# Optimization experiments

Measured on AMD Instinct MI355X. Metric: run time of the kernel, lower is better.

## Reference

```python
import jax, jax.numpy as jnp
import numpy as np

N_NODES = 50000
N_EDGES = 640000
D = 128      # in_feats
OUT = 128    # out_feats


def setup_inputs() -> dict:
    key = jax.random.key(0)
    ks = jax.random.split(key, 8)
    feat = jax.random.normal(ks[0], (N_NODES, D), dtype=jnp.float32)
    weight = jax.random.uniform(ks[1], (N_EDGES,), dtype=jnp.float32)
    src = jax.random.randint(ks[2], (N_EDGES,), 0, N_NODES, dtype=jnp.int64)
    dst = jax.random.randint(ks[3], (N_EDGES,), 0, N_NODES, dtype=jnp.int64)
    # xavier_uniform with relu gain ~ sqrt(2)*sqrt(6/(fan_in+fan_out))
    g = np.sqrt(2.0)
    lim_pool = g * np.sqrt(6.0 / (D + D))
    lim_neigh = g * np.sqrt(6.0 / (2 * D + OUT))
    W_pool = jax.random.uniform(ks[4], (D, D), dtype=jnp.float32, minval=-lim_pool, maxval=lim_pool)
    b_pool = jnp.zeros((D,), dtype=jnp.float32)
    W_neigh = jax.random.uniform(ks[5], (OUT, 2 * D), dtype=jnp.float32, minval=-lim_neigh, maxval=lim_neigh)
    b_neigh = jnp.zeros((OUT,), dtype=jnp.float32)
    return {"feat": feat, "weight": weight, "src": src, "dst": dst,
            "W_pool": W_pool, "b_pool": b_pool, "W_neigh": W_neigh, "b_neigh": b_neigh}


def reference(feat, weight, src, dst, W_pool, b_pool, W_neigh, b_neigh):
    n = feat.shape[0]
    # fc_pool: h = feat @ W_pool.T + b_pool  -> [N, D]
    h = feat @ W_pool.T + b_pool
    # u_mul_e: per-edge message m_e = h[src_e] * w_e  -> [E, D]
    m = h[src] * weight[:, None]
    # max reduce over incoming edges (scatter-max by dst)
    neigh = jax.ops.segment_max(m, dst, num_segments=n)
    # zero-degree nodes get 0 (segment_max fills empties with -inf)
    deg = jax.ops.segment_sum(jnp.ones_like(weight), dst, num_segments=n)
    neigh = jnp.where(deg[:, None] > 0, neigh, jnp.zeros((), dtype=feat.dtype))
    # fc_neigh on concat(feat, neigh)
    rst = jnp.concatenate([feat, neigh], axis=1) @ W_neigh.T + b_neigh
    return rst
```

## Files before the change

### kernel.cpp

```cpp
#include <hip/hip_runtime.h>
#include <cstdint>
#include <cstddef>

#define N_NODES 50000
#define N_EDGES 640000
#define DF 128

#define NBUCK 196
#define BCAP  6144
#define PA_BLOCKS 250

typedef __attribute__((ext_vector_type(8))) short bf16x8;
typedef __attribute__((ext_vector_type(4))) float f32x4;

__device__ inline unsigned short f2bf(float f) {
    unsigned int u = __float_as_uint(f);
    return (unsigned short)((u + 0x7fffu + ((u >> 16) & 1u)) >> 16);
}

#define NF4 (N_NODES * DF / 4)
#define NWG (3 * 2048)
__global__ __launch_bounds__(256) void k1_setup_bucket(
    const float* __restrict__ feat,
    const float* __restrict__ W_pool,
    const float* __restrict__ W_neigh,
    const int* __restrict__ src,
    const int* __restrict__ dst,
    const float* __restrict__ w,
    unsigned short* __restrict__ featb,
    unsigned short* __restrict__ Wp_f,
    unsigned short* __restrict__ Wn1_f,
    unsigned short* __restrict__ Wn2_f,
    int* __restrict__ bucketcnt,
    uint2* __restrict__ staging)
{
    int bid = blockIdx.x;
    int t = threadIdx.x;
    if (bid < PA_BLOCKS) {
        __shared__ int cnt[NBUCK];
        __shared__ int runbase[NBUCK];
        int base = bid * 2560;
        if (t < NBUCK) cnt[t] = 0;
        __syncthreads();
        uint2 rec[10];
        int bk[10];
        #pragma unroll
        for (int i = 0; i < 10; ++i) {
            int e = base + i * 256 + t;
            int s = src[e], d = dst[e];
            bk[i] = d >> 8;
            rec[i].x = (unsigned int)s | ((unsigned int)(d & 255) << 16);
            rec[i].y = __float_as_uint(w[e]);
            atomicAdd(&cnt[bk[i]], 1);
        }
        __syncthreads();
        if (t < NBUCK) {
            runbase[t] = atomicAdd(&bucketcnt[t], cnt[t]);
            cnt[t] = 0;
        }
        __syncthreads();
        #pragma unroll
        for (int i = 0; i < 10; ++i) {
            int r = atomicAdd(&cnt[bk[i]], 1);
            int pos = runbase[bk[i]] + r;
            if (pos < BCAP) staging[bk[i] * BCAP + pos] = rec[i];
        }
    } else if (bid < 250 + NF4 / 256) {
        int idx = (bid - PA_BLOCKS) * 256 + t;
        float4 v = ((const float4*)feat)[idx];
        ushort4 o;
        o.x = f2bf(v.x); o.y = f2bf(v.y); o.z = f2bf(v.z); o.w = f2bf(v.w);
        ((ushort4*)featb)[idx] = o;
    } else {
        int g = (bid - PA_BLOCKS - NF4 / 256) * 256 + t;
        int m = g >> 11;
        int r8 = g & 2047;
        int L = r8 & 63, tt = (r8 >> 6) & 3, c = r8 >> 8;
        int o = c * 16 + (L & 15);
        int kb = tt * 32 + (L >> 4) * 8;
        const float* srcp;
        unsigned short* dstp;
        if (m == 0)      { srcp = W_pool  + o * 128 + kb;       dstp = Wp_f;  }
        else if (m == 1) { srcp = W_neigh + o * 256 + kb;       dstp = Wn1_f; }
        else             { srcp = W_neigh + o * 256 + 128 + kb; dstp = Wn2_f; }
        ushort4 lo, hi;
        float4 a = ((const float4*)srcp)[0];
        float4 b = ((const float4*)srcp)[1];
        lo.x = f2bf(a.x); lo.y = f2bf(a.y); lo.z = f2bf(a.z); lo.w = f2bf(a.w);
        hi.x = f2bf(b.x); hi.y = f2bf(b.y); hi.z = f2bf(b.z); hi.w = f2bf(b.w);
        ((ushort4*)(dstp + r8 * 8))[0] = lo;
        ((ushort4*)(dstp + r8 * 8))[1] = hi;
    }
}

#define GEMMB 196
__global__ __launch_bounds__(1024) void k2_gemm_passb(
    const unsigned short* __restrict__ featb,
    const unsigned short* __restrict__ Wp_f,
    const float* __restrict__ b_pool,
    unsigned short* __restrict__ hb,
    const int* __restrict__ bucketcnt,
    const uint2* __restrict__ staging,
    int* __restrict__ offsets,
    uint2* __restrict__ edges)
{
    int t = threadIdx.x;
    if (blockIdx.x < GEMMB) {
        int wave = blockIdx.x * 16 + (t >> 6);
        int lane = t & 63;
        int m0 = wave * 16;
        if (m0 >= N_NODES) return;
        const int n = lane & 15, quad = lane >> 4;

        f32x4 acc[8];
        #pragma unroll
        for (int c = 0; c < 8; ++c) {
            float bv = b_pool[c * 16 + n];
            acc[c] = (f32x4){bv, bv, bv, bv};
        }
        const unsigned short* aptr = featb + (size_t)(m0 + n) * DF + quad * 8;
        #pragma unroll
        for (int tt = 0; tt < 4; ++tt) {
            bf16x8 af = *(const bf16x8*)(aptr + tt * 32);
            #pragma unroll
            for (int c = 0; c < 8; ++c) {
                bf16x8 bf = *(const bf16x8*)(Wp_f + (size_t)((c * 4 + tt) * 64 + lane) * 8);
                acc[c] = __builtin_amdgcn_mfma_f32_16x16x32_bf16(af, bf, acc[c], 0, 0, 0);
            }
        }
        #pragma unroll
        for (int c = 0; c < 8; ++c)
            #pragma unroll
            for (int r = 0; r < 4; ++r)
                hb[(size_t)(m0 + quad * 4 + r) * DF + c * 16 + n] = f2bf(acc[c][r]);
    } else {
        __shared__ int dcnt[256];
        __shared__ int sc[256];
        __shared__ int bc[256];
        int b = blockIdx.x - GEMMB;

        if (t < 256) { dcnt[t] = 0; bc[t] = (t < NBUCK) ? bucketcnt[t] : 0; sc[t] = (t < NBUCK) ? bc[t] : 0; }
        __syncthreads();
        #pragma unroll
        for (int off = 1; off < 256; off <<= 1) {
            int u = (t < 256 && t >= off) ? sc[t - off] : 0;
            __syncthreads();
            if (t < 256) sc[t] += u;
            __syncthreads();
        }
        int mybase = (b > 0) ? sc[b - 1] : 0;
        int cnt = bc[b];
        __syncthreads();

        uint2 rec[6];
        int nit = (cnt + 1023) >> 10;
        for (int i = 0; i < nit; ++i) {
            int idx = i * 1024 + t;
            if (idx < cnt) {
                rec[i] = staging[(size_t)b * BCAP + idx];
                atomicAdd(&dcnt[(rec[i].x >> 16) & 255], 1);
            }
        }
        __syncthreads();
        if (t < 256) sc[t] = dcnt[t];
        __syncthreads();
        #pragma unroll
        for (int off = 1; off < 256; off <<= 1) {
            int u = (t < 256 && t >= off) ? sc[t - off] : 0;
            __syncthreads();
            if (t < 256) sc[t] += u;
            __syncthreads();
        }
        if (t < 256) {
            int node = b * 256 + t;
            int excl = sc[t] - dcnt[t];
            if (node < N_NODES) offsets[node] = mybase + excl;
            dcnt[t] = mybase + excl;
        }
        if (b == NBUCK - 1 && t == 0) offsets[N_NODES] = mybase + cnt;
        __syncthreads();
        for (int i = 0; i < nit; ++i) {
            int idx = i * 1024 + t;
            if (idx < cnt) {
                int dl = (rec[i].x >> 16) & 255;
                int pos = atomicAdd(&dcnt[dl], 1);
                uint2 fin;
                fin.x = rec[i].x & 0xFFFFu;
                fin.y = rec[i].y;
                edges[pos] = fin;
            }
        }
    }
}

__global__ __launch_bounds__(256) void fused_max_out(
    const unsigned short* __restrict__ featb,
    const unsigned short* __restrict__ hb,
    const int* __restrict__ offsets,
    const uint2* __restrict__ edges,
    const unsigned short* __restrict__ Wn1_f,
    const unsigned short* __restrict__ Wn2_f,
    const float* __restrict__ bias,
    float* __restrict__ out)
{
    __shared__ __align__(16) unsigned short nsh[16 * DF];
    const int t = threadIdx.x;
    const int lane = t & 63;
    const int m0 = blockIdx.x * 16;
    const int half = lane >> 5;
    const int q = lane & 31;

    #pragma unroll 1
    for (int j = 0; j < 4; ++j) {
        const int row = ((t >> 6) << 2) + j;
        const int node = __builtin_amdgcn_readfirstlane(m0 + row);
        int beg = offsets[node], end = offsets[node + 1];
        float4 mx = make_float4(-3.4e38f, -3.4e38f, -3.4e38f, -3.4e38f);

        for (int e = beg; e < end; e += 8) {
            int i1 = min(e + 1, end - 1);
            int i2 = min(e + 2, end - 1);
            int i3 = min(e + 3, end - 1);
            int i4 = min(e + 4, end - 1);
            int i5 = min(e + 5, end - 1);
            int i6 = min(e + 6, end - 1);
            int i7 = min(e + 7, end - 1);
            uint2 e0 = edges[e],  e1 = edges[i1], e2 = edges[i2], e3 = edges[i3];
            uint2 e4 = edges[i4], e5 = edges[i5], e6 = edges[i6], e7 = edges[i7];
            uint2 mA = half ? e1 : e0;
            uint2 mB = half ? e3 : e2;
            uint2 mC = half ? e5 : e4;
            uint2 mD = half ? e7 : e6;
            float wA = __uint_as_float(mA.y);
            float wB = __uint_as_float(mB.y);
            float wC = __uint_as_float(mC.y);
            float wD = __uint_as_float(mD.y);
            uint2 pA = *(const uint2*)(hb + (size_t)mA.x * DF + q * 4);
            uint2 pB = *(const uint2*)(hb + (size_t)mB.x * DF + q * 4);
            uint2 pC = *(const uint2*)(hb + (size_t)mC.x * DF + q * 4);
            uint2 pD = *(const uint2*)(hb + (size_t)mD.x * DF + q * 4);
            mx.x = fmaxf(mx.x, __uint_as_float(pA.x << 16)          * wA);
            mx.y = fmaxf(mx.y, __uint_as_float(pA.x & 0xffff0000u)  * wA);
            mx.z = fmaxf(mx.z, __uint_as_float(pA.y << 16)          * wA);
            mx.w = fmaxf(mx.w, __uint_as_float(pA.y & 0xffff0000u)  * wA);
            mx.x = fmaxf(mx.x, __uint_as_float(pB.x << 16)          * wB);
            mx.y = fmaxf(mx.y, __uint_as_float(pB.x & 0xffff0000u)  * wB);
            mx.z = fmaxf(mx.z, __uint_as_float(pB.y << 16)          * wB);
            mx.w = fmaxf(mx.w, __uint_as_float(pB.y & 0xffff0000u)  * wB);
            mx.x = fmaxf(mx.x, __uint_as_float(pC.x << 16)          * wC);
            mx.y = fmaxf(mx.y, __uint_as_float(pC.x & 0xffff0000u)  * wC);
            mx.z = fmaxf(mx.z, __uint_as_float(pC.y << 16)          * wC);
            mx.w = fmaxf(mx.w, __uint_as_float(pC.y & 0xffff0000u)  * wC);
            mx.x = fmaxf(mx.x, __uint_as_float(pD.x << 16)          * wD);
            mx.y = fmaxf(mx.y, __uint_as_float(pD.x & 0xffff0000u)  * wD);
            mx.z = fmaxf(mx.z, __uint_as_float(pD.y << 16)          * wD);
            mx.w = fmaxf(mx.w, __uint_as_float(pD.y & 0xffff0000u)  * wD);
        }

        float4 o;
        o.x = fmaxf(mx.x, __shfl_xor(mx.x, 32));
        o.y = fmaxf(mx.y, __shfl_xor(mx.y, 32));
        o.z = fmaxf(mx.z, __shfl_xor(mx.z, 32));
        o.w = fmaxf(mx.w, __shfl_xor(mx.w, 32));
        if (beg == end) o = make_float4(0.f, 0.f, 0.f, 0.f);
        if (half == 0) {
            ushort4 ob;
            ob.x = f2bf(o.x); ob.y = f2bf(o.y); ob.z = f2bf(o.z); ob.w = f2bf(o.w);
            int boff = row * 256 + ((q * 8) ^ ((row & 7) << 4));
            *(ushort4*)((char*)nsh + boff) = ob;
        }
    }

    const int n = lane & 15, quad = lane >> 4;
    f32x4 acc[8];
    #pragma unroll
    for (int c = 0; c < 8; ++c) {
        float bv = bias[c * 16 + n];
        acc[c] = (f32x4){bv, bv, bv, bv};
    }

    const unsigned short* a0 = featb + (size_t)(m0 + n) * DF + quad * 8;
    #pragma unroll
    for (int tt = 0; tt < 4; ++tt) {
        bf16x8 af = *(const bf16x8*)(a0 + tt * 32);
        #pragma unroll
        for (int c = 0; c < 8; ++c) {
            bf16x8 bfv = *(const bf16x8*)(Wn1_f + (size_t)((c * 4 + tt) * 64 + lane) * 8);
            acc[c] = __builtin_amdgcn_mfma_f32_16x16x32_bf16(af, bfv, acc[c], 0, 0, 0);
        }
    }

    __syncthreads();

    #pragma unroll
    for (int tt = 0; tt < 4; ++tt) {
        int boff = (quad * 16 + tt * 64) ^ ((n & 7) << 4);
        bf16x8 af = *(const bf16x8*)((const char*)nsh + n * 256 + boff);
        #pragma unroll
        for (int c = 0; c < 8; ++c) {
            bf16x8 bfv = *(const bf16x8*)(Wn2_f + (size_t)((c * 4 + tt) * 64 + lane) * 8);
            acc[c] = __builtin_amdgcn_mfma_f32_16x16x32_bf16(af, bfv, acc[c], 0, 0, 0);
        }
    }

    #pragma unroll
    for (int c = 0; c < 8; ++c)
        #pragma unroll
        for (int r = 0; r < 4; ++r)
            out[(size_t)(m0 + quad * 4 + r) * DF + c * 16 + n] = acc[c][r];
}

extern "C" void kernel_launch(void* const* d_in, const int* in_sizes, int n_in,
                              void* d_out, int out_size, void* d_ws, size_t ws_size,
                              hipStream_t stream) {
    const float* feat    = (const float*)d_in[0];
    const float* weight  = (const float*)d_in[1];
    const int*   src     = (const int*)d_in[2];
    const int*   dst     = (const int*)d_in[3];
    const float* W_pool  = (const float*)d_in[4];
    const float* b_pool  = (const float*)d_in[5];
    const float* W_neigh = (const float*)d_in[6];
    const float* b_neigh = (const float*)d_in[7];
    float* out = (float*)d_out;

    char* ws = (char*)d_ws;
    unsigned short* featb  = (unsigned short*)(ws);
    unsigned short* hb     = (unsigned short*)(ws + 12800000);
    unsigned short* Wp_f   = (unsigned short*)(ws + 38400000);
    unsigned short* Wn1_f  = (unsigned short*)(ws + 38432768);
    unsigned short* Wn2_f  = (unsigned short*)(ws + 38465536);
    int*   offsets   = (int*)  (ws + 38498304);
    int*   bucketcnt = (int*)  (ws + 38698368);
    uint2* staging   = (uint2*)(ws + 38699392);
    uint2* edges     = (uint2*)(ws + 48333184);

    hipMemsetAsync(bucketcnt, 0, 1024, stream);

    const int K1_BLOCKS = PA_BLOCKS + NF4 / 256 + NWG / 256;
    k1_setup_bucket<<<K1_BLOCKS, 256, 0, stream>>>(
        feat, W_pool, W_neigh, src, dst, weight,
        featb, Wp_f, Wn1_f, Wn2_f, bucketcnt, staging);

    k2_gemm_passb<<<GEMMB + NBUCK, 1024, 0, stream>>>(
        featb, Wp_f, b_pool, hb, bucketcnt, staging, offsets, edges);

    fused_max_out<<<N_NODES / 16, 256, 0, stream>>>(
        featb, hb, offsets, edges, Wn1_f, Wn2_f, b_neigh, out);
}
```

Baseline: 193.5 us.

## Use one wave per node in fused max-aggregate kernel with 1024-thread blocks

The fused gather-max/output kernel now launches 1024-thread blocks so each of the 16 waves handles one destination node's max aggregation, where before each wave looped over four nodes. The output GEMM is split so that the first 8 waves each compute one 16-column tile of the output, while the other waves exit after the barrier. This exposes more memory-level parallelism in the irregular gather and shortens the serial per-wave loop. The cost is idle waves during the MFMA phase and larger blocks, which may limit occupancy and scheduling flexibility.

Result: faster. 163.4 us (-15.6%).

```diff
diff --git a/kernel.cpp b/kernel.cpp
--- a/kernel.cpp
+++ b/kernel.cpp
@@ -193,7 +193,7 @@
     }
 }
 
-__global__ __launch_bounds__(256) void fused_max_out(
+__global__ __launch_bounds__(1024) void fused_max_out(
     const unsigned short* __restrict__ featb,
     const unsigned short* __restrict__ hb,
     const int* __restrict__ offsets,
@@ -206,108 +206,98 @@
     __shared__ __align__(16) unsigned short nsh[16 * DF];
     const int t = threadIdx.x;
     const int lane = t & 63;
+    const int wid = t >> 6;
     const int m0 = blockIdx.x * 16;
     const int half = lane >> 5;
     const int q = lane & 31;
 
-    #pragma unroll 1
-    for (int j = 0; j < 4; ++j) {
-        const int row = ((t >> 6) << 2) + j;
-        const int node = __builtin_amdgcn_readfirstlane(m0 + row);
-        int beg = offsets[node], end = offsets[node + 1];
-        float4 mx = make_float4(-3.4e38f, -3.4e38f, -3.4e38f, -3.4e38f);
-
-        for (int e = beg; e < end; e += 8) {
-            int i1 = min(e + 1, end - 1);
-            int i2 = min(e + 2, end - 1);
-            int i3 = min(e + 3, end - 1);
-            int i4 = min(e + 4, end - 1);
-            int i5 = min(e + 5, end - 1);
-            int i6 = min(e + 6, end - 1);
-            int i7 = min(e + 7, end - 1);
-            uint2 e0 = edges[e],  e1 = edges[i1], e2 = edges[i2], e3 = edges[i3];
-            uint2 e4 = edges[i4], e5 = edges[i5], e6 = edges[i6], e7 = edges[i7];
-            uint2 mA = half ? e1 : e0;
-            uint2 mB = half ? e3 : e2;
-            uint2 mC = half ? e5 : e4;
-            uint2 mD = half ? e7 : e6;
-            float wA = __uint_as_float(mA.y);
-            float wB = __uint_as_float(mB.y);
-            float wC = __uint_as_float(mC.y);
-            float wD = __uint_as_float(mD.y);
-            uint2 pA = *(const uint2*)(hb + (size_t)mA.x * DF + q * 4);
-            uint2 pB = *(const uint2*)(hb + (size_t)mB.x * DF + q * 4);
-            uint2 pC = *(const uint2*)(hb + (size_t)mC.x * DF + q * 4);
-            uint2 pD = *(const uint2*)(hb + (size_t)mD.x * DF + q * 4);
-            mx.x = fmaxf(mx.x, __uint_as_float(pA.x << 16)          * wA);
-            mx.y = fmaxf(mx.y, __uint_as_float(pA.x & 0xffff0000u)  * wA);
-            mx.z = fmaxf(mx.z, __uint_as_float(pA.y << 16)          * wA);
-            mx.w = fmaxf(mx.w, __uint_as_float(pA.y & 0xffff0000u)  * wA);
-            mx.x = fmaxf(mx.x, __uint_as_float(pB.x << 16)          * wB);
-            mx.y = fmaxf(mx.y, __uint_as_float(pB.x & 0xffff0000u)  * wB);
-            mx.z = fmaxf(mx.z, __uint_as_float(pB.y << 16)          * wB);
-            mx.w = fmaxf(mx.w, __uint_as_float(pB.y & 0xffff0000u)  * wB);
-            mx.x = fmaxf(mx.x, __uint_as_float(pC.x << 16)          * wC);
-            mx.y = fmaxf(mx.y, __uint_as_float(pC.x & 0xffff0000u)  * wC);
-            mx.z = fmaxf(mx.z, __uint_as_float(pC.y << 16)          * wC);
-            mx.w = fmaxf(mx.w, __uint_as_float(pC.y & 0xffff0000u)  * wC);
-            mx.x = fmaxf(mx.x, __uint_as_float(pD.x << 16)          * wD);
-            mx.y = fmaxf(mx.y, __uint_as_float(pD.x & 0xffff0000u)  * wD);
-            mx.z = fmaxf(mx.z, __uint_as_float(pD.y << 16)          * wD);
-            mx.w = fmaxf(mx.w, __uint_as_float(pD.y & 0xffff0000u)  * wD);
-        }
-
-        float4 o;
-        o.x = fmaxf(mx.x, __shfl_xor(mx.x, 32));
-        o.y = fmaxf(mx.y, __shfl_xor(mx.y, 32));
-        o.z = fmaxf(mx.z, __shfl_xor(mx.z, 32));
-        o.w = fmaxf(mx.w, __shfl_xor(mx.w, 32));
-        if (beg == end) o = make_float4(0.f, 0.f, 0.f, 0.f);
-        if (half == 0) {
-            ushort4 ob;
-            ob.x = f2bf(o.x); ob.y = f2bf(o.y); ob.z = f2bf(o.z); ob.w = f2bf(o.w);
-            int boff = row * 256 + ((q * 8) ^ ((row & 7) << 4));
-            *(ushort4*)((char*)nsh + boff) = ob;
-        }
+    const int node = __builtin_amdgcn_readfirstlane(m0 + wid);
+    int beg = offsets[node], end = offsets[node + 1];
+    float4 mx = make_float4(-3.4e38f, -3.4e38f, -3.4e38f, -3.4e38f);
+
+    for (int e = beg; e < end; e += 8) {
+        int i1 = min(e + 1, end - 1);
+        int i2 = min(e + 2, end - 1);
+        int i3 = min(e + 3, end - 1);
+        int i4 = min(e + 4, end - 1);
+        int i5 = min(e + 5, end - 1);
+        int i6 = min(e + 6, end - 1);
+        int i7 = min(e + 7, end - 1);
+        uint2 e0 = edges[e],  e1 = edges[i1], e2 = edges[i2], e3 = edges[i3];
+        uint2 e4 = edges[i4], e5 = edges[i5], e6 = edges[i6], e7 = edges[i7];
+        uint2 mA = half ? e1 : e0;
+        uint2 mB = half ? e3 : e2;
+        uint2 mC = half ? e5 : e4;
+        uint2 mD = half ? e7 : e6;
+        float wA = __uint_as_float(mA.y);
+        float wB = __uint_as_float(mB.y);
+        float wC = __uint_as_float(mC.y);
+        float wD = __uint_as_float(mD.y);
+        uint2 pA = *(const uint2*)(hb + (size_t)mA.x * DF + q * 4);
+        uint2 pB = *(const uint2*)(hb + (size_t)mB.x * DF + q * 4);
+        uint2 pC = *(const uint2*)(hb + (size_t)mC.x * DF + q * 4);
+        uint2 pD = *(const uint2*)(hb + (size_t)mD.x * DF + q * 4);
+        mx.x = fmaxf(mx.x, __uint_as_float(pA.x << 16)          * wA);
+        mx.y = fmaxf(mx.y, __uint_as_float(pA.x & 0xffff0000u)  * wA);
+        mx.z = fmaxf(mx.z, __uint_as_float(pA.y << 16)          * wA);
+        mx.w = fmaxf(mx.w, __uint_as_float(pA.y & 0xffff0000u)  * wA);
+        mx.x = fmaxf(mx.x, __uint_as_float(pB.x << 16)          * wB);
+        mx.y = fmaxf(mx.y, __uint_as_float(pB.x & 0xffff0000u)  * wB);
+        mx.z = fmaxf(mx.z, __uint_as_float(pB.y << 16)          * wB);
+        mx.w = fmaxf(mx.w, __uint_as_float(pB.y & 0xffff0000u)  * wB);
+        mx.x = fmaxf(mx.x, __uint_as_float(pC.x << 16)          * wC);
+        mx.y = fmaxf(mx.y, __uint_as_float(pC.x & 0xffff0000u)  * wC);
+        mx.z = fmaxf(mx.z, __uint_as_float(pC.y << 16)          * wC);
+        mx.w = fmaxf(mx.w, __uint_as_float(pC.y & 0xffff0000u)  * wC);
+        mx.x = fmaxf(mx.x, __uint_as_float(pD.x << 16)          * wD);
+        mx.y = fmaxf(mx.y, __uint_as_float(pD.x & 0xffff0000u)  * wD);
+        mx.z = fmaxf(mx.z, __uint_as_float(pD.y << 16)          * wD);
+        mx.w = fmaxf(mx.w, __uint_as_float(pD.y & 0xffff0000u)  * wD);
+    }
+
+    float4 o;
+    o.x = fmaxf(mx.x, __shfl_xor(mx.x, 32));
+    o.y = fmaxf(mx.y, __shfl_xor(mx.y, 32));
+    o.z = fmaxf(mx.z, __shfl_xor(mx.z, 32));
+    o.w = fmaxf(mx.w, __shfl_xor(mx.w, 32));
+    if (beg == end) o = make_float4(0.f, 0.f, 0.f, 0.f);
+    if (half == 0) {
+        ushort4 ob;
+        ob.x = f2bf(o.x); ob.y = f2bf(o.y); ob.z = f2bf(o.z); ob.w = f2bf(o.w);
+        int boff = wid * 256 + ((q * 8) ^ ((wid & 7) << 4));
+        *(ushort4*)((char*)nsh + boff) = ob;
     }
 
     const int n = lane & 15, quad = lane >> 4;
-    f32x4 acc[8];
-    #pragma unroll
-    for (int c = 0; c < 8; ++c) {
+    f32x4 acc;
+    if (wid < 8) {
+        const int c = wid;
         float bv = bias[c * 16 + n];
-        acc[c] = (f32x4){bv, bv, bv, bv};
-    }
-
-    const unsigned short* a0 = featb + (size_t)(m0 + n) * DF + quad * 8;
-    #pragma unroll
-    for (int tt = 0; tt < 4; ++tt) {
-        bf16x8 af = *(const bf16x8*)(a0 + tt * 32);
-        #pragma unroll
-        for (int c = 0; c < 8; ++c) {
+        acc = (f32x4){bv, bv, bv, bv};
+        const unsigned short* a0 = featb + (size_t)(m0 + n) * DF + quad * 8;
+        #pragma unroll
+        for (int tt = 0; tt < 4; ++tt) {
+            bf16x8 af = *(const bf16x8*)(a0 + tt * 32);
             bf16x8 bfv = *(const bf16x8*)(Wn1_f + (size_t)((c * 4 + tt) * 64 + lane) * 8);
-            acc[c] = __builtin_amdgcn_mfma_f32_16x16x32_bf16(af, bfv, acc[c], 0, 0, 0);
+            acc = __builtin_amdgcn_mfma_f32_16x16x32_bf16(af, bfv, acc, 0, 0, 0);
         }
     }
 
     __syncthreads();
-
+    if (wid >= 8) return;
+
+    const int c = wid;
     #pragma unroll
     for (int tt = 0; tt < 4; ++tt) {
         int boff = (quad * 16 + tt * 64) ^ ((n & 7) << 4);
         bf16x8 af = *(const bf16x8*)((const char*)nsh + n * 256 + boff);
-        #pragma unroll
-        for (int c = 0; c < 8; ++c) {
-            bf16x8 bfv = *(const bf16x8*)(Wn2_f + (size_t)((c * 4 + tt) * 64 + lane) * 8);
-            acc[c] = __builtin_amdgcn_mfma_f32_16x16x32_bf16(af, bfv, acc[c], 0, 0, 0);
-        }
+        bf16x8 bfv = *(const bf16x8*)(Wn2_f + (size_t)((c * 4 + tt) * 64 + lane) * 8);
+        acc = __builtin_amdgcn_mfma_f32_16x16x32_bf16(af, bfv, acc, 0, 0, 0);
     }
 
     #pragma unroll
-    for (int c = 0; c < 8; ++c)
-        #pragma unroll
-        for (int r = 0; r < 4; ++r)
-            out[(size_t)(m0 + quad * 4 + r) * DF + c * 16 + n] = acc[c][r];
+    for (int r = 0; r < 4; ++r)
+        out[(size_t)(m0 + quad * 4 + r) * DF + c * 16 + n] = acc[r];
 }
 
 extern "C" void kernel_launch(void* const* d_in, const int* in_sizes, int n_in,
@@ -344,6 +334,6 @@
     k2_gemm_passb<<<GEMMB + NBUCK, 1024, 0, stream>>>(
         featb, Wp_f, b_pool, hb, bucketcnt, staging, offsets, edges);
 
-    fused_max_out<<<N_NODES / 16, 256, 0, stream>>>(
+    fused_max_out<<<N_NODES / 16, 1024, 0, stream>>>(
         featb, hb, offsets, edges, Wn1_f, Wn2_f, b_neigh, out);
 }
```

## Pad per-node edge lists to multiples of 8 and split max-aggregation from output GEMM

Applied to the files above, without the earlier changes.

Each node's edge list is padded to a multiple of 8 with dummy edges that point at a sentinel hb row holding a very negative value. This removes the per-iteration min() index clamping in the gather loop. Buckets get a fixed ECAP-sized edge region, so the cross-bucket prefix scan is no longer needed. The fused max+GEMM kernel is split into a one-wave-per-node max kernel that writes a bf16 neigh buffer, followed by a separate MFMA GEMM kernel. The split adds an extra launch plus a round trip of the neigh buffer through global memory, and padding adds gather traffic on the sentinel row.

Measured after the change: 162.3 us. 16.1% less time.

```diff
diff --git a/kernel.cpp b/kernel.cpp
--- a/kernel.cpp
+++ b/kernel.cpp
@@ -8,7 +8,9 @@
 
 #define NBUCK 196
 #define BCAP  6144
+#define ECAP  8192
 #define PA_BLOCKS 250
+#define DUMMY_ROW 50000
 
 typedef __attribute__((ext_vector_type(8))) short bf16x8;
 typedef __attribute__((ext_vector_type(4))) float f32x4;
@@ -28,6 +30,7 @@
     const int* __restrict__ dst,
     const float* __restrict__ w,
     unsigned short* __restrict__ featb,
+    unsigned short* __restrict__ hb,
     unsigned short* __restrict__ Wp_f,
     unsigned short* __restrict__ Wn1_f,
     unsigned short* __restrict__ Wn2_f,
@@ -71,7 +74,7 @@
         ushort4 o;
         o.x = f2bf(v.x); o.y = f2bf(v.y); o.z = f2bf(v.z); o.w = f2bf(v.w);
         ((ushort4*)featb)[idx] = o;
-    } else {
+    } else if (bid < 250 + NF4 / 256 + NWG / 256) {
         int g = (bid - PA_BLOCKS - NF4 / 256) * 256 + t;
         int m = g >> 11;
         int r8 = g & 2047;
@@ -90,6 +93,8 @@
         hi.x = f2bf(b.x); hi.y = f2bf(b.y); hi.z = f2bf(b.z); hi.w = f2bf(b.w);
         ((ushort4*)(dstp + r8 * 8))[0] = lo;
         ((ushort4*)(dstp + r8 * 8))[1] = hi;
+    } else {
+        if (t < DF) hb[(size_t)DUMMY_ROW * DF + t] = 0xFF7Fu;
     }
 }
 
@@ -102,6 +107,7 @@
     const int* __restrict__ bucketcnt,
     const uint2* __restrict__ staging,
     int* __restrict__ offsets,
+    int* __restrict__ nend,
     uint2* __restrict__ edges)
 {
     int t = threadIdx.x;
@@ -136,20 +142,11 @@
     } else {
         __shared__ int dcnt[256];
         __shared__ int sc[256];
-        __shared__ int bc[256];
         int b = blockIdx.x - GEMMB;
-
-        if (t < 256) { dcnt[t] = 0; bc[t] = (t < NBUCK) ? bucketcnt[t] : 0; sc[t] = (t < NBUCK) ? bc[t] : 0; }
-        __syncthreads();
-        #pragma unroll
-        for (int off = 1; off < 256; off <<= 1) {
-            int u = (t < 256 && t >= off) ? sc[t - off] : 0;
-            __syncthreads();
-            if (t < 256) sc[t] += u;
-            __syncthreads();
-        }
-        int mybase = (b > 0) ? sc[b - 1] : 0;
-        int cnt = bc[b];
+        int cnt = bucketcnt[b];
+        if (cnt > BCAP) cnt = BCAP;
+
+        if (t < 256) dcnt[t] = 0;
         __syncthreads();
 
         uint2 rec[6];
@@ -162,7 +159,12 @@
             }
         }
         __syncthreads();
-        if (t < 256) sc[t] = dcnt[t];
+        int mydeg = 0, mypad = 0;
+        if (t < 256) {
+            mydeg = dcnt[t];
+            mypad = (mydeg + 7) & ~7;
+            sc[t] = mypad;
+        }
         __syncthreads();
         #pragma unroll
         for (int off = 1; off < 256; off <<= 1) {
@@ -172,12 +174,16 @@
             __syncthreads();
         }
         if (t < 256) {
+            int beg = b * ECAP + sc[t] - mypad;
             int node = b * 256 + t;
-            int excl = sc[t] - dcnt[t];
-            if (node < N_NODES) offsets[node] = mybase + excl;
-            dcnt[t] = mybase + excl;
-        }
-        if (b == NBUCK - 1 && t == 0) offsets[N_NODES] = mybase + cnt;
+            if (node < N_NODES) {
+                offsets[node] = beg;
+                nend[node] = beg + mypad;
+            }
+            dcnt[t] = beg;
+            uint2 dmy; dmy.x = DUMMY_ROW; dmy.y = 0x3F800000u;
+            for (int k = mydeg; k < mypad; ++k) edges[beg + k] = dmy;
+        }
         __syncthreads();
         for (int i = 0; i < nit; ++i) {
             int idx = i * 1024 + t;
@@ -193,85 +199,82 @@
     }
 }
 
-__global__ __launch_bounds__(256) void fused_max_out(
+__global__ __launch_bounds__(256) void neigh_max_kernel(
+    const unsigned short* __restrict__ hb, const int* __restrict__ offsets,
+    const int* __restrict__ nend,
+    const uint2* __restrict__ edges,
+    unsigned short* __restrict__ neighb)
+{
+    int gwave = (blockIdx.x * 256 + threadIdx.x) >> 6;
+    if (gwave >= N_NODES) return;
+    int node = __builtin_amdgcn_readfirstlane(gwave);
+    int lane = threadIdx.x & 63;
+    const int half = lane >> 5;
+    const int q = lane & 31;
+
+    int beg = offsets[node], end = nend[node];
+    float4 acc = make_float4(-3.4e38f, -3.4e38f, -3.4e38f, -3.4e38f);
+
+    for (int e = beg; e < end; e += 8) {
+        uint2 e0 = edges[e],     e1 = edges[e + 1], e2 = edges[e + 2], e3 = edges[e + 3];
+        uint2 e4 = edges[e + 4], e5 = edges[e + 5], e6 = edges[e + 6], e7 = edges[e + 7];
+        uint2 mA = half ? e1 : e0;
+        uint2 mB = half ? e3 : e2;
+        uint2 mC = half ? e5 : e4;
+        uint2 mD = half ? e7 : e6;
+        float wA = __uint_as_float(mA.y);
+        float wB = __uint_as_float(mB.y);
+        float wC = __uint_as_float(mC.y);
+        float wD = __uint_as_float(mD.y);
+        uint2 pA = *(const uint2*)(hb + (size_t)mA.x * DF + q * 4);
+        uint2 pB = *(const uint2*)(hb + (size_t)mB.x * DF + q * 4);
+        uint2 pC = *(const uint2*)(hb + (size_t)mC.x * DF + q * 4);
+        uint2 pD = *(const uint2*)(hb + (size_t)mD.x * DF + q * 4);
+        acc.x = fmaxf(acc.x, __uint_as_float(pA.x << 16)          * wA);
+        acc.y = fmaxf(acc.y, __uint_as_float(pA.x & 0xffff0000u)  * wA);
+        acc.z = fmaxf(acc.z, __uint_as_float(pA.y << 16)          * wA);
+        acc.w = fmaxf(acc.w, __uint_as_float(pA.y & 0xffff0000u)  * wA);
+        acc.x = fmaxf(acc.x, __uint_as_float(pB.x << 16)          * wB);
+        acc.y = fmaxf(acc.y, __uint_as_float(pB.x & 0xffff0000u)  * wB);
+        acc.z = fmaxf(acc.z, __uint_as_float(pB.y << 16)          * wB);
+        acc.w = fmaxf(acc.w, __uint_as_float(pB.y & 0xffff0000u)  * wB);
+        acc.x = fmaxf(acc.x, __uint_as_float(pC.x << 16)          * wC);
+        acc.y = fmaxf(acc.y, __uint_as_float(pC.x & 0xffff0000u)  * wC);
+        acc.z = fmaxf(acc.z, __uint_as_float(pC.y << 16)          * wC);
+        acc.w = fmaxf(acc.w, __uint_as_float(pC.y & 0xffff0000u)  * wC);
+        acc.x = fmaxf(acc.x, __uint_as_float(pD.x << 16)          * wD);
+        acc.y = fmaxf(acc.y, __uint_as_float(pD.x & 0xffff0000u)  * wD);
+        acc.z = fmaxf(acc.z, __uint_as_float(pD.y << 16)          * wD);
+        acc.w = fmaxf(acc.w, __uint_as_float(pD.y & 0xffff0000u)  * wD);
+    }
+
+    float4 o;
+    o.x = fmaxf(acc.x, __shfl_xor(acc.x, 32));
+    o.y = fmaxf(acc.y, __shfl_xor(acc.y, 32));
+    o.z = fmaxf(acc.z, __shfl_xor(acc.z, 32));
+    o.w = fmaxf(acc.w, __shfl_xor(acc.w, 32));
+    if (beg == end) o = make_float4(0.f, 0.f, 0.f, 0.f);
+    if (half == 0) {
+        ushort4 ob;
+        ob.x = f2bf(o.x); ob.y = f2bf(o.y); ob.z = f2bf(o.z); ob.w = f2bf(o.w);
+        *(ushort4*)(neighb + (size_t)node * DF + q * 4) = ob;
+    }
+}
+
+__global__ __launch_bounds__(256) void gemm_out(
     const unsigned short* __restrict__ featb,
-    const unsigned short* __restrict__ hb,
-    const int* __restrict__ offsets,
-    const uint2* __restrict__ edges,
+    const unsigned short* __restrict__ neighb,
     const unsigned short* __restrict__ Wn1_f,
     const unsigned short* __restrict__ Wn2_f,
     const float* __restrict__ bias,
     float* __restrict__ out)
 {
-    __shared__ __align__(16) unsigned short nsh[16 * DF];
-    const int t = threadIdx.x;
-    const int lane = t & 63;
-    const int m0 = blockIdx.x * 16;
-    const int half = lane >> 5;
-    const int q = lane & 31;
-
-    #pragma unroll 1
-    for (int j = 0; j < 4; ++j) {
-        const int row = ((t >> 6) << 2) + j;
-        const int node = __builtin_amdgcn_readfirstlane(m0 + row);
-        int beg = offsets[node], end = offsets[node + 1];
-        float4 mx = make_float4(-3.4e38f, -3.4e38f, -3.4e38f, -3.4e38f);
-
-        for (int e = beg; e < end; e += 8) {
-            int i1 = min(e + 1, end - 1);
-            int i2 = min(e + 2, end - 1);
-            int i3 = min(e + 3, end - 1);
-            int i4 = min(e + 4, end - 1);
-            int i5 = min(e + 5, end - 1);
-            int i6 = min(e + 6, end - 1);
-            int i7 = min(e + 7, end - 1);
-            uint2 e0 = edges[e],  e1 = edges[i1], e2 = edges[i2], e3 = edges[i3];
-            uint2 e4 = edges[i4], e5 = edges[i5], e6 = edges[i6], e7 = edges[i7];
-            uint2 mA = half ? e1 : e0;
-            uint2 mB = half ? e3 : e2;
-            uint2 mC = half ? e5 : e4;
-            uint2 mD = half ? e7 : e6;
-            float wA = __uint_as_float(mA.y);
-            float wB = __uint_as_float(mB.y);
-            float wC = __uint_as_float(mC.y);
-            float wD = __uint_as_float(mD.y);
-            uint2 pA = *(const uint2*)(hb + (size_t)mA.x * DF + q * 4);
-            uint2 pB = *(const uint2*)(hb + (size_t)mB.x * DF + q * 4);
-            uint2 pC = *(const uint2*)(hb + (size_t)mC.x * DF + q * 4);
-            uint2 pD = *(const uint2*)(hb + (size_t)mD.x * DF + q * 4);
-            mx.x = fmaxf(mx.x, __uint_as_float(pA.x << 16)          * wA);
-            mx.y = fmaxf(mx.y, __uint_as_float(pA.x & 0xffff0000u)  * wA);
-            mx.z = fmaxf(mx.z, __uint_as_float(pA.y << 16)          * wA);
-            mx.w = fmaxf(mx.w, __uint_as_float(pA.y & 0xffff0000u)  * wA);
-            mx.x = fmaxf(mx.x, __uint_as_float(pB.x << 16)          * wB);
-            mx.y = fmaxf(mx.y, __uint_as_float(pB.x & 0xffff0000u)  * wB);
-            mx.z = fmaxf(mx.z, __uint_as_float(pB.y << 16)          * wB);
-            mx.w = fmaxf(mx.w, __uint_as_float(pB.y & 0xffff0000u)  * wB);
-            mx.x = fmaxf(mx.x, __uint_as_float(pC.x << 16)          * wC);
-            mx.y = fmaxf(mx.y, __uint_as_float(pC.x & 0xffff0000u)  * wC);
-            mx.z = fmaxf(mx.z, __uint_as_float(pC.y << 16)          * wC);
-            mx.w = fmaxf(mx.w, __uint_as_float(pC.y & 0xffff0000u)  * wC);
-            mx.x = fmaxf(mx.x, __uint_as_float(pD.x << 16)          * wD);
-            mx.y = fmaxf(mx.y, __uint_as_float(pD.x & 0xffff0000u)  * wD);
-            mx.z = fmaxf(mx.z, __uint_as_float(pD.y << 16)          * wD);
-            mx.w = fmaxf(mx.w, __uint_as_float(pD.y & 0xffff0000u)  * wD);
-        }
-
-        float4 o;
-        o.x = fmaxf(mx.x, __shfl_xor(mx.x, 32));
-        o.y = fmaxf(mx.y, __shfl_xor(mx.y, 32));
-        o.z = fmaxf(mx.z, __shfl_xor(mx.z, 32));
-        o.w = fmaxf(mx.w, __shfl_xor(mx.w, 32));
-        if (beg == end) o = make_float4(0.f, 0.f, 0.f, 0.f);
-        if (half == 0) {
-            ushort4 ob;
-            ob.x = f2bf(o.x); ob.y = f2bf(o.y); ob.z = f2bf(o.z); ob.w = f2bf(o.w);
-            int boff = row * 256 + ((q * 8) ^ ((row & 7) << 4));
-            *(ushort4*)((char*)nsh + boff) = ob;
-        }
-    }
-
+    int wave = (blockIdx.x * 256 + threadIdx.x) >> 6;
+    int lane = threadIdx.x & 63;
+    int m0 = wave * 16;
+    if (m0 >= N_NODES) return;
     const int n = lane & 15, quad = lane >> 4;
+
     f32x4 acc[8];
     #pragma unroll
     for (int c = 0; c < 8; ++c) {
@@ -279,27 +282,24 @@
         acc[c] = (f32x4){bv, bv, bv, bv};
     }
 
-    const unsigned short* a0 = featb + (size_t)(m0 + n) * DF + quad * 8;
+    const unsigned short* a0 = featb  + (size_t)(m0 + n) * DF + quad * 8;
+    const unsigned short* a1 = neighb + (size_t)(m0 + n) * DF + quad * 8;
     #pragma unroll
-    for (int tt = 0; tt < 4; ++tt) {
-        bf16x8 af = *(const bf16x8*)(a0 + tt * 32);
+    for (int t = 0; t < 4; ++t) {
+        bf16x8 af = *(const bf16x8*)(a0 + t * 32);
         #pragma unroll
         for (int c = 0; c < 8; ++c) {
-            bf16x8 bfv = *(const bf16x8*)(Wn1_f + (size_t)((c * 4 + tt) * 64 + lane) * 8);
-            acc[c] = __builtin_amdgcn_mfma_f32_16x16x32_bf16(af, bfv, acc[c], 0, 0, 0);
-        }
-    }
-
-    __syncthreads();
-
+            bf16x8 bf = *(const bf16x8*)(Wn1_f + (size_t)((c * 4 + t) * 64 + lane) * 8);
+            acc[c] = __builtin_amdgcn_mfma_f32_16x16x32_bf16(af, bf, acc[c], 0, 0, 0);
+        }
+    }
     #pragma unroll
-    for (int tt = 0; tt < 4; ++tt) {
-        int boff = (quad * 16 + tt * 64) ^ ((n & 7) << 4);
-        bf16x8 af = *(const bf16x8*)((const char*)nsh + n * 256 + boff);
+    for (int t = 0; t < 4; ++t) {
+        bf16x8 af = *(const bf16x8*)(a1 + t * 32);
         #pragma unroll
         for (int c = 0; c < 8; ++c) {
-            bf16x8 bfv = *(const bf16x8*)(Wn2_f + (size_t)((c * 4 + tt) * 64 + lane) * 8);
-            acc[c] = __builtin_amdgcn_mfma_f32_16x16x32_bf16(af, bfv, acc[c], 0, 0, 0);
+            bf16x8 bf = *(const bf16x8*)(Wn2_f + (size_t)((c * 4 + t) * 64 + lane) * 8);
+            acc[c] = __builtin_amdgcn_mfma_f32_16x16x32_bf16(af, bf, acc[c], 0, 0, 0);
         }
     }
 
@@ -326,24 +326,29 @@
     char* ws = (char*)d_ws;
     unsigned short* featb  = (unsigned short*)(ws);
     unsigned short* hb     = (unsigned short*)(ws + 12800000);
-    unsigned short* Wp_f   = (unsigned short*)(ws + 38400000);
-    unsigned short* Wn1_f  = (unsigned short*)(ws + 38432768);
-    unsigned short* Wn2_f  = (unsigned short*)(ws + 38465536);
-    int*   offsets   = (int*)  (ws + 38498304);
-    int*   bucketcnt = (int*)  (ws + 38698368);
-    uint2* staging   = (uint2*)(ws + 38699392);
-    uint2* edges     = (uint2*)(ws + 48333184);
+    unsigned short* Wp_f   = (unsigned short*)(ws + 25600512);
+    unsigned short* Wn1_f  = (unsigned short*)(ws + 25633280);
+    unsigned short* Wn2_f  = (unsigned short*)(ws + 25666048);
+    int*   offsets   = (int*)  (ws + 25698816);
+    int*   nend      = (int*)  (ws + 25898816);
+    int*   bucketcnt = (int*)  (ws + 26098816);
+    uint2* staging   = (uint2*)(ws + 26099840);
+    uint2* edges     = (uint2*)(ws + 35733632);
+    unsigned short* neighb = (unsigned short*)(ws + 48578688);
 
     hipMemsetAsync(bucketcnt, 0, 1024, stream);
 
-    const int K1_BLOCKS = PA_BLOCKS + NF4 / 256 + NWG / 256;
+    const int K1_BLOCKS = PA_BLOCKS + NF4 / 256 + NWG / 256 + 1;
     k1_setup_bucket<<<K1_BLOCKS, 256, 0, stream>>>(
         feat, W_pool, W_neigh, src, dst, weight,
-        featb, Wp_f, Wn1_f, Wn2_f, bucketcnt, staging);
+        featb, hb, Wp_f, Wn1_f, Wn2_f, bucketcnt, staging);
 
     k2_gemm_passb<<<GEMMB + NBUCK, 1024, 0, stream>>>(
-        featb, Wp_f, b_pool, hb, bucketcnt, staging, offsets, edges);
-
-    fused_max_out<<<N_NODES / 16, 256, 0, stream>>>(
-        featb, hb, offsets, edges, Wn1_f, Wn2_f, b_neigh, out);
-}
+        featb, Wp_f, b_pool, hb, bucketcnt, staging, offsets, nend, edges);
+
+    neigh_max_kernel<<<(N_NODES + 3) / 4, 256, 0, stream>>>(
+        hb, offsets, nend, edges, neighb);
+
+    gemm_out<<<782, 256, 0, stream>>>(
+        featb, neighb, Wn1_f, Wn2_f, b_neigh, out);
+}
```
